# Kernel tuning notes

Measured on AMD Instinct MI355X. Metric: run time of the kernel, lower is better.

## Reference

```python
import jax, jax.numpy as jnp
import numpy as np

N = 8192      # atoms
E = 131072    # edges (avg degree 16)
C = 32        # channels per irrep
Z = 10        # num_elements
G = 16        # num_graphs
NB = 8        # num_bessel
NSH = 9       # spherical harmonic components for max_ell=2 (1+3+5)
R_MAX = 5.0
P_CUT = 5     # num_polynomial_cutoff
AVG_NEIGH = 16.0
LMAP = np.array([0, 1, 1, 1, 2, 2, 2, 2, 2])  # m-component -> l index


def _sph(u):
    # real spherical harmonics up to l=2, 'component' normalization, unit input
    x, y, z = u[:, 0], u[:, 1], u[:, 2]
    s3, s5, s15 = 3.0 ** 0.5, 5.0 ** 0.5, 15.0 ** 0.5
    return jnp.stack([
        jnp.ones_like(x),
        s3 * x, s3 * y, s3 * z,
        s15 * x * y, s15 * y * z, (s5 / 2) * (3 * z * z - 1.0),
        s15 * x * z, (s15 / 2) * (x * x - y * y),
    ], axis=1)  # [E, 9]


def _radial(r):
    # Bessel radial basis with smooth polynomial cutoff (MACE RadialEmbeddingBlock)
    n = jnp.arange(1, NB + 1, dtype=r.dtype)  # [NB]
    pref = (2.0 / R_MAX) ** 0.5
    bessel = pref * jnp.sin(n[None, :] * jnp.pi * r[:, None] / R_MAX) / r[:, None]
    x = r / R_MAX
    p = float(P_CUT)
    env = (1.0 - (p + 1.0) * (p + 2.0) / 2.0 * x ** P_CUT
           + p * (p + 2.0) * x ** (P_CUT + 1)
           - p * (p + 1.0) / 2.0 * x ** (P_CUT + 2))
    env = env * (x < 1.0)
    return bessel * env[:, None]  # [E, NB]


def setup_inputs() -> dict:
    key = jax.random.key(0)
    k = jax.random.split(key, 24)
    positions = jax.random.normal(k[0], (N, 3), dtype=jnp.float32) * 2.0
    species = jax.random.randint(k[1], (N,), 0, Z)
    node_attrs = jax.nn.one_hot(species, Z, dtype=jnp.float32)
    edge_index = jax.random.randint(k[2], (2, E), 0, N, dtype=jnp.int32)
    batch = jnp.sort(jax.random.randint(k[3], (N,), 0, G, dtype=jnp.int32))
    charges = jax.random.normal(k[4], (N,), dtype=jnp.float32) * 0.1
    sd = 0.1
    atomic_energies = jax.random.normal(k[5], (Z,), dtype=jnp.float32)
    W_embed = jax.random.normal(k[6], (Z, C), dtype=jnp.float32) * sd
    R0 = jax.random.normal(k[7], (2, NB, 64), dtype=jnp.float32) / np.sqrt(NB)
    R1 = jax.random.normal(k[8], (2, 64, 64), dtype=jnp.float32) / 8.0
    R2 = jax.random.normal(k[9], (2, 64, 64), dtype=jnp.float32) / 8.0
    R3 = jax.random.normal(k[10], (2, 64, 3 * C), dtype=jnp.float32) / 8.0
    W_mix = jax.random.normal(k[11], (2, 3, C, C), dtype=jnp.float32) / np.sqrt(C)
    W_sc = jax.random.normal(k[12], (2, 3, C, C), dtype=jnp.float32) / np.sqrt(C)
    Wp1 = jax.random.normal(k[13], (2, Z, C), dtype=jnp.float32) * 0.5
    Wp2 = jax.random.normal(k[14], (2, Z, C), dtype=jnp.float32) * 0.5
    Wp3 = jax.random.normal(k[15], (2, Z, C), dtype=jnp.float32) * 0.5
    wE1 = jax.random.normal(k[16], (C,), dtype=jnp.float32) * sd
    wD1 = jax.random.normal(k[17], (C,), dtype=jnp.float32) * sd
    Wh = jax.random.normal(k[18], (C, 16), dtype=jnp.float32) / np.sqrt(C)
    wE2 = jax.random.normal(k[19], (16,), dtype=jnp.float32) * sd
    wD2 = jax.random.normal(k[20], (C,), dtype=jnp.float32) * sd
    return dict(positions=positions, node_attrs=node_attrs, charges=charges,
                atomic_energies=atomic_energies, W_embed=W_embed,
                R0=R0, R1=R1, R2=R2, R3=R3, W_mix=W_mix, W_sc=W_sc,
                Wp1=Wp1, Wp2=Wp2, Wp3=Wp3, wE1=wE1, wD1=wD1, Wh=Wh,
                wE2=wE2, wD2=wD2, edge_index=edge_index, batch=batch)


def reference(positions, node_attrs, charges, atomic_energies, W_embed,
              R0, R1, R2, R3, W_mix, W_sc, Wp1, Wp2, Wp3,
              wE1, wD1, Wh, wE2, wD2, edge_index, batch):
    snd, rcv = edge_index[0], edge_index[1]
    lmap = jnp.asarray(LMAP)

    # edge geometry
    vec = positions[rcv] - positions[snd]          # [E,3]
    r = jnp.sqrt(jnp.sum(vec * vec, axis=1) + 1e-12)
    Y = _sph(vec / r[:, None])                     # [E,9]
    rb = _radial(r)                                # [E,NB]

    # atomic reference energies e0
    node_e0 = node_attrs @ atomic_energies         # [N]
    e_tot = jax.ops.segment_sum(node_e0, batch, num_segments=G)

    # node embedding (scalar channels), lifted into full irrep layout [N,9,C]
    h0 = node_attrs @ W_embed
    h = jnp.zeros((N, NSH, C), h0.dtype).at[:, 0, :].set(h0)

    dip = jnp.zeros((N, 3), positions.dtype)
    for i in range(2):
        # radial MLP -> per-edge, per-l tensor-product weights
        x = jax.nn.silu(rb @ R0[i])
        x = jax.nn.silu(x @ R1[i])
        x = jax.nn.silu(x @ R2[i])
        Rw = (x @ R3[i]).reshape(E, 3, C)[:, lmap, :]       # [E,9,C]
        # edge-wise tensor product: scalar node feats x SH, radially weighted
        hs = h[:, 0, :]                                      # [N,C]
        msg = Rw * Y[:, :, None] * hs[snd][:, None, :]       # [E,9,C]
        # scatter-sum message passing
        A = jax.ops.segment_sum(msg, rcv, num_segments=N) / AVG_NEIGH
        A = jnp.einsum('nmc,mcd->nmd', A, W_mix[i][lmap])    # per-l linear
        sc = jnp.einsum('nmc,mcd->nmd', h, W_sc[i][lmap])    # self-connection
        # symmetric product basis (correlation 3, element-dependent weights)
        s = A[:, 0, :]
        w1 = node_attrs @ Wp1[i]
        w2 = node_attrs @ Wp2[i]
        w3 = node_attrs @ Wp3[i]
        B = A * (w1[:, None, :] + w2[:, None, :] * s[:, None, :]
                 + w3[:, None, :] * (s * s)[:, None, :])
        h = B + sc
        # readouts: energy from 0e channels, dipole from 1o channels
        if i == 0:
            e_node = h[:, 0, :] @ wE1
            d_node = jnp.einsum('nmc,c->nm', h[:, 1:4, :], wD1)
        else:
            hid = jax.nn.silu(h[:, 0, :] @ Wh)
            e_node = hid @ wE2
            d_node = jnp.einsum('nmc,c->nm', h[:, 1:4, :], wD2)
        e_tot = e_tot + jax.ops.segment_sum(e_node, batch, num_segments=G)
        dip = dip + d_node

    total_dipole = jax.ops.segment_sum(dip, batch, num_segments=G)
    total_dipole = total_dipole + jax.ops.segment_sum(
        charges[:, None] * positions, batch, num_segments=G)  # fixed-charge baseline
    return jnp.concatenate([e_tot[:, None], total_dipole], axis=1)  # [G,4]
```

## Files before the change

kernel.cpp:

```cpp
#include <hip/hip_runtime.h>
#include <math.h>

#define N_NODES 8192
#define N_EDGES 131072
#define C 32
#define Zn 10
#define NG 16
#define NB 8
#define H 64
#define TABN 4096
#define TPP 16
#define NPB 8
#define CAP 64
#define SL 48

#define TB_TAB  514
#define TB_EDGE (TB_TAB + 512)
#define TB_H0   (TB_EDGE + 128)

__device__ __forceinline__ float silu_f(float v){ return v / (1.0f + __expf(-v)); }

__global__ __launch_bounds__(256)
void prep_kernel(const float* __restrict__ pos, const int* __restrict__ ei,
                 int* __restrict__ cursor, int* __restrict__ bucket,
                 const float* __restrict__ na, const float* __restrict__ Wemb,
                 int* __restrict__ species, float* __restrict__ hg,
                 const float* __restrict__ R0g, const float* __restrict__ R1g,
                 const float* __restrict__ R2g, const float* __restrict__ R3g,
                 float2* __restrict__ Tab2, float* __restrict__ out){
  __shared__ float xsh[TPP*65];
  __shared__ int spec_lds[64];
  int b = blockIdx.x;
  int tid = threadIdx.x;

  if (b >= TB_TAB){
    if (b < TB_EDGE){
      int e = (b-TB_TAB)*256 + tid;
      int snd = ei[e], rcv = ei[N_EDGES + e];
      float px = pos[rcv*3+0]-pos[snd*3+0];
      float py = pos[rcv*3+1]-pos[snd*3+1];
      float pz = pos[rcv*3+2]-pos[snd*3+2];
      float r2 = px*px+py*py+pz*pz;
      if (r2 < 25.0f){
        int slot = atomicAdd(cursor + rcv, 1);
        if (slot < CAP) bucket[rcv*CAP + slot] = snd;
      }
    } else {
      int n0 = (b-TB_EDGE)*64;
      if (tid < 64){
        int n = n0 + tid;
        int spec = 0;
        #pragma unroll
        for (int z = 1; z < Zn; z++) if (na[n*Zn+z] > 0.5f) spec = z;
        species[n] = spec;
        spec_lds[tid] = spec;
      }
      if (b == TB_EDGE && tid >= 64 && tid < 128) out[tid-64] = 0.f;
      __syncthreads();
      float4* dst = (float4*)(hg + (size_t)n0*288);
      const float4 z4 = make_float4(0.f,0.f,0.f,0.f);
      #pragma unroll
      for (int it = 0; it < 18; it++){
        int f = it*256 + tid;
        int node = f / 72;
        int q = f - node*72;
        float4 v = z4;
        if (q < 8) v = ((const float4*)(Wemb + spec_lds[node]*C))[q];
        dst[f] = v;
      }
    }
    return;
  }

  const int nb = 257;
  int half = (b >= nb) ? 1 : 0;
  int blk  = b - half*nb;
  const float* R0i = R0g + half*NB*H;
  const float* R1i = R1g + half*H*H;
  const float* R2i = R2g + half*H*H;
  const float* R3i = R3g + half*H*96;
  float2* TabH = Tab2 + (size_t)half*((size_t)TABN*96);

  int pl = tid >> 4, jt = tid & 15;
  int i = blk*TPP + pl;
  float r = (i == 0) ? 1e-6f : (float)i * (5.0f/TABN);
  if (jt < 8){
    float xr = r*0.2f;
    float env = 0.f;
    if (xr < 1.0f){
      float x2 = xr*xr, x5 = x2*x2*xr;
      env = 1.f - 21.f*x5 + 35.f*x5*xr - 15.f*x5*x2;
    }
    float sc = 0.6324555320336759f / r * env;
    xsh[pl*65 + jt] = sc * sinf((float)(jt+1)*0.6283185307179586f*r);
  }
  __syncthreads();

  float acc[6];
  #pragma unroll
  for (int j = 0; j < 4; j++) acc[j] = 0.f;
  #pragma unroll
  for (int k = 0; k < 8; k++){
    float xk = xsh[pl*65 + k];
    float4 w = *(const float4*)(R0i + k*H + jt*4);
    acc[0]=fmaf(xk,w.x,acc[0]); acc[1]=fmaf(xk,w.y,acc[1]);
    acc[2]=fmaf(xk,w.z,acc[2]); acc[3]=fmaf(xk,w.w,acc[3]);
  }
  __syncthreads();
  #pragma unroll
  for (int j = 0; j < 4; j++) xsh[pl*65 + jt*4 + j] = silu_f(acc[j]);
  __syncthreads();

  const float* Wl[2] = {R1i, R2i};
  #pragma unroll
  for (int L = 0; L < 2; L++){
    const float* W = Wl[L];
    #pragma unroll
    for (int j = 0; j < 4; j++) acc[j] = 0.f;
    #pragma unroll 8
    for (int k = 0; k < H; k++){
      float xk = xsh[pl*65 + k];
      float4 w = *(const float4*)(W + k*H + jt*4);
      acc[0]=fmaf(xk,w.x,acc[0]); acc[1]=fmaf(xk,w.y,acc[1]);
      acc[2]=fmaf(xk,w.z,acc[2]); acc[3]=fmaf(xk,w.w,acc[3]);
    }
    __syncthreads();
    #pragma unroll
    for (int j = 0; j < 4; j++) xsh[pl*65 + jt*4 + j] = silu_f(acc[j]);
    __syncthreads();
  }

  #pragma unroll
  for (int j = 0; j < 6; j++) acc[j] = 0.f;
  #pragma unroll 8
  for (int k = 0; k < H; k++){
    float xk = xsh[pl*65 + k];
    const float* wp = R3i + k*96 + jt*6;
    float2 w0 = *(const float2*)(wp);
    float2 w1 = *(const float2*)(wp+2);
    float2 w2 = *(const float2*)(wp+4);
    acc[0]=fmaf(xk,w0.x,acc[0]); acc[1]=fmaf(xk,w0.y,acc[1]);
    acc[2]=fmaf(xk,w1.x,acc[2]); acc[3]=fmaf(xk,w1.y,acc[3]);
    acc[4]=fmaf(xk,w2.x,acc[4]); acc[5]=fmaf(xk,w2.y,acc[5]);
  }
  if (i <= TABN){
    int cb = jt*6;
    #pragma unroll
    for (int j = 0; j < 6; j++){
      int c = cb + j;
      float val = acc[j];
      if (i < TABN) TabH[(size_t)i*96 + c].x = val;
      if (i > 0)    TabH[(size_t)(i-1)*96 + c].y = val;
    }
  }
}

__global__ __launch_bounds__(512)
void node_kernel(const float2* __restrict__ Tab2, const int* __restrict__ bucket,
                 const int* __restrict__ deg,
                 const float* __restrict__ hg_in, float* __restrict__ hg_out,
                 const float* __restrict__ Wm_g, const float* __restrict__ Ws_g,
                 const float* __restrict__ Wp1, const float* __restrict__ Wp2,
                 const float* __restrict__ Wp3,
                 const int* __restrict__ species, const int* __restrict__ batch,
                 const float* __restrict__ ae, const float* __restrict__ charges,
                 const float* __restrict__ pos,
                 const float* __restrict__ wEv, const float* __restrict__ wDv,
                 const float* __restrict__ Whg, const float* __restrict__ wE2g,
                 int iter, float* __restrict__ out){
  __shared__ float WmT[3*32*34];
  __shared__ float WsT[3*32*34];
  __shared__ float abuf[NPB][288];
  __shared__ float sbuf[NPB][288];
  __shared__ float estage[NPB][SL][6];
  __shared__ float glds[NG][4];
  int tid = threadIdx.x;
  for (int t = tid; t < 3072; t += 512){
    int l = t >> 10, rem = t & 1023, c = rem >> 5, d = rem & 31;
    WmT[(l*32+d)*34 + c] = Wm_g[t];
    WsT[(l*32+d)*34 + c] = Ws_g[t];
  }
  if (tid < NG*4) glds[tid>>2][tid&3] = 0.f;
  int w = tid >> 6, lane = tid & 63;
  int c31 = lane & 31;
  bool hi = lane >= 32;
  int ng0 = blockIdx.x*NPB;
  int n = ng0 + w;

  int cnt = deg[n]; if (cnt > SL) cnt = SL;
  if (lane < cnt){
    int snd = bucket[n*CAP + lane];
    float px = pos[n*3+0] - pos[snd*3+0];
    float py = pos[n*3+1] - pos[snd*3+1];
    float pz = pos[n*3+2] - pos[snd*3+2];
    float r = sqrtf(px*px+py*py+pz*pz + 1e-12f);
    float inv = 1.0f/r;
    float* es = &estage[w][lane][0];
    es[0] = px*inv; es[1] = py*inv; es[2] = pz*inv;
    es[3] = r * (TABN/5.0f);
    es[4] = __int_as_float(snd);
  }

  const float s3 = 1.7320508075688772f;
  const float s5 = 2.23606797749979f;
  const float s15 = 3.872983346207417f;
  int colA = (hi ? 32 : 0) + c31;
  int colB = 32 + c31;
  int colC = 64 + c31;
  float acc0=0.f, acc1=0.f, acc2=0.f, acc3=0.f, acc4=0.f;
  #pragma unroll 4
  for (int j = 0; j < cnt; j++){
    const float* es = &estage[w][j][0];
    float x = es[0], y = es[1], z = es[2], u = es[3];
    int snd = __float_as_int(es[4]);
    int i0 = (int)u;
    if (i0 > TABN-1) i0 = TABN-1;
    float f = u - (float)i0;
    const float2* T2 = Tab2 + (size_t)i0*96;
    float hs = hg_in[(size_t)snd*288 + c31];
    float2 ta = T2[colA];
    float2 tb = T2[colB];
    float2 tc = T2[colC];
    float wv0 = fmaf(ta.y - ta.x, f, ta.x) * hs;
    float wv1 = fmaf(tb.y - tb.x, f, tb.x) * hs;
    float wv2 = fmaf(tc.y - tc.x, f, tc.x) * hs;
    float Ys0 = hi ? s3*x : 1.0f;
    float Ys1 = s3 * (hi ? z : y);
    float Ys2 = s15 * (hi ? y*z : x*y);
    float Ys3 = hi ? s15*x*z : 0.5f*s5*(3.f*z*z - 1.f);
    float Ys4 = 0.5f*s15*(x*x - y*y);
    acc0 = fmaf(wv0, Ys0, acc0);
    acc1 = fmaf(wv1, Ys1, acc1);
    acc2 = fmaf(wv2, Ys2, acc2);
    acc3 = fmaf(wv2, Ys3, acc3);
    acc4 = fmaf(wv2, Ys4, acc4);
  }
  abuf[w][lane]       = acc0 * (1.0f/16.0f);
  abuf[w][lane + 64]  = acc1 * (1.0f/16.0f);
  abuf[w][lane + 128] = acc2 * (1.0f/16.0f);
  abuf[w][lane + 192] = acc3 * (1.0f/16.0f);
  if (!hi) abuf[w][lane + 256] = acc4 * (1.0f/16.0f);
  __syncthreads();

  float a2[NPB], scv[NPB];
  int idx0 = w*64 + lane;
  bool actm = (w < 5) && (idx0 < 288);
  if (w < 5){
    int m = idx0 >> 5; if (m > 8) m = 8;
    int l = (m >= 4) ? 2 : ((m >= 1) ? 1 : 0);
    const float* wmB = WmT + (l*32 + c31)*34;
    const float* wsB = WsT + (l*32 + c31)*34;
    #pragma unroll
    for (int n2 = 0; n2 < NPB; n2++){ a2[n2] = 0.f; scv[n2] = 0.f; }
    #pragma unroll
    for (int q = 0; q < 8; q++){
      float2 wa0 = *(const float2*)(wmB + 4*q);
      float2 wa1 = *(const float2*)(wmB + 4*q + 2);
      float2 sa0 = *(const float2*)(wsB + 4*q);
      float2 sa1 = *(const float2*)(wsB + 4*q + 2);
      #pragma unroll
      for (int n2 = 0; n2 < NPB; n2++){
        float4 av = *(const float4*)(&abuf[n2][m*32 + 4*q]);
        float4 hv = *(const float4*)(hg_in + (size_t)(ng0+n2)*288 + m*32 + 4*q);
        a2[n2] = fmaf(av.x, wa0.x, a2[n2]); a2[n2] = fmaf(av.y, wa0.y, a2[n2]);
        a2[n2] = fmaf(av.z, wa1.x, a2[n2]); a2[n2] = fmaf(av.w, wa1.y, a2[n2]);
        scv[n2] = fmaf(hv.x, sa0.x, scv[n2]); scv[n2] = fmaf(hv.y, sa0.y, scv[n2]);
        scv[n2] = fmaf(hv.z, sa1.x, scv[n2]); scv[n2] = fmaf(hv.w, sa1.y, scv[n2]);
      }
    }
  }
  __syncthreads();
  if (actm){
    #pragma unroll
    for (int n2 = 0; n2 < NPB; n2++){
      abuf[n2][idx0] = a2[n2];
      sbuf[n2][idx0] = scv[n2];
    }
  }
  __syncthreads();

  int spec = species[n];
  float sval = abuf[w][c31];
  float p1 = Wp1[spec*C+c31], p2 = Wp2[spec*C+c31], p3 = Wp3[spec*C+c31];
  float f = p1 + p2*sval + p3*sval*sval;
  #pragma unroll
  for (int it = 0; it < 5; it++){
    int idx = it*64 + lane;
    if (idx < 288){
      float hn = abuf[w][idx]*f + sbuf[w][idx];
      hg_out[(size_t)n*288 + idx] = hn;
      abuf[w][idx] = hn;
    }
  }

  int g = batch[n];
  float dv0 = 0.f, dv1 = 0.f, dv2 = 0.f, ev = 0.f;
  if (lane < 32){
    dv0 = abuf[w][32+lane]*wDv[lane];
    dv1 = abuf[w][64+lane]*wDv[lane];
    dv2 = abuf[w][96+lane]*wDv[lane];
  }
  if (iter == 0){
    if (lane < 32) ev = abuf[w][lane]*wEv[lane];
  } else {
    if (lane < 16){
      float hid = 0.f;
      #pragma unroll
      for (int c = 0; c < 32; c++) hid = fmaf(abuf[w][c], Whg[c*16+lane], hid);
      hid = silu_f(hid);
      ev = hid * wE2g[lane];
    }
  }
  #pragma unroll
  for (int off = 16; off >= 1; off >>= 1){
    ev  += __shfl_down(ev,  off);
    dv0 += __shfl_down(dv0, off);
    dv1 += __shfl_down(dv1, off);
    dv2 += __shfl_down(dv2, off);
  }
  if (lane == 0){
    if (iter == 0){
      ev += ae[spec];
      float q = charges[n];
      dv0 += q*pos[n*3+0];
      dv1 += q*pos[n*3+1];
      dv2 += q*pos[n*3+2];
    }
    atomicAdd(&glds[g][0], ev);
    atomicAdd(&glds[g][1], dv0);
    atomicAdd(&glds[g][2], dv1);
    atomicAdd(&glds[g][3], dv2);
  }
  __syncthreads();
  if (tid < NG*4){
    float v = glds[tid>>2][tid&3];
    if (v != 0.f) atomicAdd(out + tid, v);
  }
}

extern "C" void kernel_launch(void* const* d_in, const int* in_sizes, int n_in,
                              void* d_out, int out_size, void* d_ws, size_t ws_size,
                              hipStream_t stream){
  const float* positions       = (const float*)d_in[0];
  const float* node_attrs      = (const float*)d_in[1];
  const float* charges         = (const float*)d_in[2];
  const float* atomic_energies = (const float*)d_in[3];
  const float* W_embed         = (const float*)d_in[4];
  const float* R0              = (const float*)d_in[5];
  const float* R1              = (const float*)d_in[6];
  const float* R2              = (const float*)d_in[7];
  const float* R3              = (const float*)d_in[8];
  const float* W_mix           = (const float*)d_in[9];
  const float* W_sc            = (const float*)d_in[10];
  const float* Wp1             = (const float*)d_in[11];
  const float* Wp2             = (const float*)d_in[12];
  const float* Wp3             = (const float*)d_in[13];
  const float* wE1             = (const float*)d_in[14];
  const float* wD1             = (const float*)d_in[15];
  const float* Wh              = (const float*)d_in[16];
  const float* wE2             = (const float*)d_in[17];
  const float* wD2             = (const float*)d_in[18];
  const int*   edge_index      = (const int*)d_in[19];
  const int*   batch           = (const int*)d_in[20];
  float* out = (float*)d_out;

  char* wsp = (char*)d_ws;
  int*    bucket = (int*)wsp;    wsp += sizeof(int)*(size_t)N_NODES*CAP;
  float2* Tab2   = (float2*)wsp; wsp += sizeof(float2)*(size_t)2*TABN*96;
  float*  hg_a   = (float*)wsp;  wsp += sizeof(float)*(size_t)N_NODES*288;
  float*  hg_b   = (float*)wsp;  wsp += sizeof(float)*(size_t)N_NODES*288;
  int* cursor    = (int*)wsp;    wsp += sizeof(int)*N_NODES;
  int* species   = (int*)wsp;    wsp += sizeof(int)*N_NODES;

  hipMemsetAsync(cursor, 0, N_NODES*sizeof(int), stream);

  prep_kernel<<<TB_H0, 256, 0, stream>>>(positions, edge_index, cursor, bucket,
                                         node_attrs, W_embed, species, hg_a,
                                         R0, R1, R2, R3, Tab2, out);

  for (int i = 0; i < 2; i++){
    const float* hin  = (i == 0) ? hg_a : hg_b;
    float*       hout = (i == 0) ? hg_b : hg_a;
    node_kernel<<<N_NODES/NPB, 512, 0, stream>>>(Tab2 + (size_t)i*TABN*96, bucket,
                                               cursor, hin, hout,
                                               W_mix + i*3*C*C, W_sc + i*3*C*C,
                                               Wp1 + i*Zn*C, Wp2 + i*Zn*C, Wp3 + i*Zn*C,
                                               species, batch,
                                               atomic_energies, charges, positions,
                                               wE1, (i == 0) ? wD1 : wD2,
                                               Wh, wE2, i, out);
  }
}
```

Measured before the change: 201.9 us.

## Split radial-table MLP over more blocks and skip final-layer feature stores

```diff
diff --git a/kernel.cpp b/kernel.cpp
--- a/kernel.cpp
+++ b/kernel.cpp
@@ -9,12 +9,12 @@
 #define NB 8
 #define H 64
 #define TABN 4096
-#define TPP 16
+#define TPP 8
 #define NPB 8
 #define CAP 64
 #define SL 48
 
-#define TB_TAB  514
+#define TB_TAB  1026
 #define TB_EDGE (TB_TAB + 512)
 #define TB_H0   (TB_EDGE + 128)
 
@@ -72,7 +72,7 @@
     return;
   }
 
-  const int nb = 257;
+  const int nb = 513;
   int half = (b >= nb) ? 1 : 0;
   int blk  = b - half*nb;
   const float* R0i = R0g + half*NB*H;
@@ -81,7 +81,7 @@
   const float* R3i = R3g + half*H*96;
   float2* TabH = Tab2 + (size_t)half*((size_t)TABN*96);
 
-  int pl = tid >> 4, jt = tid & 15;
+  int pl = tid >> 5, jt = tid & 31;
   int i = blk*TPP + pl;
   float r = (i == 0) ? 1e-6f : (float)i * (5.0f/TABN);
   if (jt < 8){
@@ -96,57 +96,49 @@
   }
   __syncthreads();
 
-  float acc[6];
-  #pragma unroll
-  for (int j = 0; j < 4; j++) acc[j] = 0.f;
+  float acc[3];
+  acc[0] = 0.f; acc[1] = 0.f;
   #pragma unroll
   for (int k = 0; k < 8; k++){
     float xk = xsh[pl*65 + k];
-    float4 w = *(const float4*)(R0i + k*H + jt*4);
+    float2 w = *(const float2*)(R0i + k*H + jt*2);
     acc[0]=fmaf(xk,w.x,acc[0]); acc[1]=fmaf(xk,w.y,acc[1]);
-    acc[2]=fmaf(xk,w.z,acc[2]); acc[3]=fmaf(xk,w.w,acc[3]);
-  }
-  __syncthreads();
-  #pragma unroll
-  for (int j = 0; j < 4; j++) xsh[pl*65 + jt*4 + j] = silu_f(acc[j]);
+  }
+  __syncthreads();
+  xsh[pl*65 + jt*2]     = silu_f(acc[0]);
+  xsh[pl*65 + jt*2 + 1] = silu_f(acc[1]);
   __syncthreads();
 
   const float* Wl[2] = {R1i, R2i};
   #pragma unroll
   for (int L = 0; L < 2; L++){
     const float* W = Wl[L];
-    #pragma unroll
-    for (int j = 0; j < 4; j++) acc[j] = 0.f;
+    acc[0] = 0.f; acc[1] = 0.f;
     #pragma unroll 8
     for (int k = 0; k < H; k++){
       float xk = xsh[pl*65 + k];
-      float4 w = *(const float4*)(W + k*H + jt*4);
+      float2 w = *(const float2*)(W + k*H + jt*2);
       acc[0]=fmaf(xk,w.x,acc[0]); acc[1]=fmaf(xk,w.y,acc[1]);
-      acc[2]=fmaf(xk,w.z,acc[2]); acc[3]=fmaf(xk,w.w,acc[3]);
     }
     __syncthreads();
-    #pragma unroll
-    for (int j = 0; j < 4; j++) xsh[pl*65 + jt*4 + j] = silu_f(acc[j]);
+    xsh[pl*65 + jt*2]     = silu_f(acc[0]);
+    xsh[pl*65 + jt*2 + 1] = silu_f(acc[1]);
     __syncthreads();
   }
 
-  #pragma unroll
-  for (int j = 0; j < 6; j++) acc[j] = 0.f;
+  acc[0] = 0.f; acc[1] = 0.f; acc[2] = 0.f;
   #pragma unroll 8
   for (int k = 0; k < H; k++){
     float xk = xsh[pl*65 + k];
-    const float* wp = R3i + k*96 + jt*6;
-    float2 w0 = *(const float2*)(wp);
-    float2 w1 = *(const float2*)(wp+2);
-    float2 w2 = *(const float2*)(wp+4);
-    acc[0]=fmaf(xk,w0.x,acc[0]); acc[1]=fmaf(xk,w0.y,acc[1]);
-    acc[2]=fmaf(xk,w1.x,acc[2]); acc[3]=fmaf(xk,w1.y,acc[3]);
-    acc[4]=fmaf(xk,w2.x,acc[4]); acc[5]=fmaf(xk,w2.y,acc[5]);
+    const float* wp = R3i + k*96 + jt*3;
+    acc[0]=fmaf(xk,wp[0],acc[0]);
+    acc[1]=fmaf(xk,wp[1],acc[1]);
+    acc[2]=fmaf(xk,wp[2],acc[2]);
   }
   if (i <= TABN){
-    int cb = jt*6;
+    int cb = jt*3;
     #pragma unroll
-    for (int j = 0; j < 6; j++){
+    for (int j = 0; j < 3; j++){
       int c = cb + j;
       float val = acc[j];
       if (i < TABN) TabH[(size_t)i*96 + c].x = val;
@@ -288,7 +280,7 @@
     int idx = it*64 + lane;
     if (idx < 288){
       float hn = abuf[w][idx]*f + sbuf[w][idx];
-      hg_out[(size_t)n*288 + idx] = hn;
+      if (iter == 0) hg_out[(size_t)n*288 + idx] = hn;
       abuf[w][idx] = hn;
     }
   }
```

Measured after the change: 200.4 us. No clear change (-0.8%).
